# Kernel tuning notes

Hardware: AMD Instinct MI355X
Metric: run time of the kernel (lower is better)

## Reference

```python
import jax, jax.numpy as jnp
import numpy as np

B, T, C, U = 128, 160, 6000, 32
BLANK = C - 1          # Keras ctc_batch_cost / tf.nn.ctc_loss: blank is last class
S = 2 * U + 1          # extended label length (blanks interleaved)
NEG = -1e30
EPS = 1e-7             # keras.backend.epsilon()


def setup_inputs() -> dict:
    key = jax.random.key(0)
    k1, k2, k3, k4 = jax.random.split(key, 4)
    logits = jax.random.normal(k1, (B, T, C), dtype=jnp.float32)
    y_pred = jax.nn.softmax(logits, axis=-1)  # ctc_batch_cost expects probabilities
    y_true = jax.random.randint(k2, (B, U), 0, C - 1)      # labels exclude blank
    input_length = jax.random.randint(k3, (B, 1), 120, T + 1)
    label_length = jax.random.randint(k4, (B, 1), 8, U + 1)
    return {"y_true": y_true, "y_pred": y_pred,
            "input_length": input_length, "label_length": label_length}


def _ctc_batch_cost(y_true, y_pred, input_length, label_length):
    # log probs, matching K.ctc_batch_cost: log(y_pred + epsilon)
    log_probs = jnp.log(y_pred + EPS)                      # [B,T,C]

    # extended label sequence: blank, l1, blank, l2, ..., blank
    ext = jnp.full((B, S), BLANK, dtype=y_true.dtype).at[:, 1::2].set(y_true)  # [B,S]
    # skip transition s-2 -> s allowed iff ext[s] != blank and ext[s] != ext[s-2]
    skip = jnp.zeros((B, S), dtype=bool)
    skip = skip.at[:, 3::2].set(y_true[:, 1:] != y_true[:, :-1])

    # per-frame log prob of each extended symbol: [B,T,S]
    lp_ext = jnp.take_along_axis(log_probs, ext[:, None, :], axis=2)

    # alpha at t=0: only positions 0 (blank) and 1 (first label)
    alpha0 = (jnp.full((B, S), NEG, dtype=log_probs.dtype)
              .at[:, 0].set(lp_ext[:, 0, 0])
              .at[:, 1].set(lp_ext[:, 0, 1]))

    def step(alpha, x):
        lp_t, t = x                                        # lp_t: [B,S]
        p1 = jnp.pad(alpha, ((0, 0), (1, 0)), constant_values=NEG)[:, :S]
        p2 = jnp.pad(alpha, ((0, 0), (2, 0)), constant_values=NEG)[:, :S]
        new = jnp.logaddexp(jnp.logaddexp(alpha, p1),
                            jnp.where(skip, p2, NEG)) + lp_t
        # freeze sequences that have run out of frames
        new = jnp.where(t < input_length, new, alpha)
        return new, None

    lp_seq = jnp.swapaxes(lp_ext, 0, 1)[1:]                # [T-1,B,S]
    ts = jnp.arange(1, T)
    alpha, _ = jax.lax.scan(step, alpha0, (lp_seq, ts))

    # total prob ends at final blank (s=2L) or final label (s=2L-1)
    end = 2 * label_length                                  # [B,1]
    a_end = jnp.take_along_axis(alpha, end, axis=1)[:, 0]
    a_end1 = jnp.take_along_axis(alpha, end - 1, axis=1)[:, 0]
    loss = -jnp.logaddexp(a_end, a_end1)
    return loss[:, None]                                    # [B,1], as in Keras


def reference(y_true, y_pred, input_length, label_length):
    return _ctc_batch_cost(y_true, y_pred, input_length, label_length)
```

## Files before the change

### kernel.cpp

```cpp
#include <hip/hip_runtime.h>
#include <math.h>

#define BB 128
#define TT 160
#define CC 6000
#define UU 32
#define SS 65
#define BLANK (CC - 1)
#define NEGV (-1e30f)
#define EPSV (1e-7f)
#define NTHR 1024

__device__ __forceinline__ float laddexp(float a, float b) {
    float m = fmaxf(a, b);
    float d = fabsf(a - b);
    return m + log1pf(expf(-d));
}

__global__ __launch_bounds__(NTHR) void ctc_loss_kernel(
    const int*   __restrict__ y_true,
    const float* __restrict__ y_pred,
    const int*   __restrict__ input_length,
    const int*   __restrict__ label_length,
    float*       __restrict__ out)
{
    __shared__ float lpb[TT];
    __shared__ float lpl[TT * UU];
    __shared__ int   yt[UU];

    const int b   = blockIdx.x;
    const int tid = threadIdx.x;

    if (tid < UU) yt[tid] = y_true[b * UU + tid];
    __syncthreads();

    const int len = input_length[b];
    const int L   = label_length[b];

    const float* yp = y_pred + (size_t)b * TT * CC;
    for (int t = tid; t < len; t += NTHR)
        lpb[t] = logf(yp[t * CC + BLANK] + EPSV);
    const int nl = len * UU;
    for (int idx = tid; idx < nl; idx += NTHR) {
        int t = idx >> 5;
        int u = idx & 31;
        lpl[idx] = logf(yp[t * CC + yt[u]] + EPSV);
    }
    __syncthreads();

    if (tid >= 64) return;
    const int  lane = tid;
    const bool odd  = lane & 1;
    const int  u    = lane >> 1;

    const bool skip = odd && (lane >= 3) && (yt[u] != yt[u - 1]);

    {
        float v0 = odd ? lpl[0] : lpb[0];
        float a = (lane <= 1) ? v0 : NEGV;
        float a64 = NEGV;

        float lpB_cur = lpb[1];
        float lp_cur  = odd ? lpl[UU + u] : lpB_cur;

        for (int t = 1; t < len; ++t) {
            int tn = (t + 1 < len) ? t + 1 : t;
            float lpB_nxt = lpb[tn];
            float lp_nxt  = odd ? lpl[tn * UU + u] : lpB_nxt;

            float a63 = __shfl(a, 63);
            float p1  = __shfl_up(a, 1);
            float p2  = __shfl_up(a, 2);
            if (lane < 1) p1 = NEGV;
            if (lane < 2) p2 = NEGV;

            float nv  = laddexp(laddexp(a, p1), skip ? p2 : NEGV) + lp_cur;
            float n64 = laddexp(a64, a63) + lpB_cur;

            a   = nv;
            a64 = n64;
            lp_cur  = lp_nxt;
            lpB_cur = lpB_nxt;
        }

        const int e = 2 * L;
        float ae  = (e == 64) ? a64 : __shfl(a, e);
        float ae1 = __shfl(a, e - 1);

        if (lane == 0) out[b] = -laddexp(ae, ae1);
    }
}

extern "C" void kernel_launch(void* const* d_in, const int* in_sizes, int n_in,
                              void* d_out, int out_size, void* d_ws, size_t ws_size,
                              hipStream_t stream) {
    const int*   y_true       = (const int*)  d_in[0];
    const float* y_pred       = (const float*)d_in[1];
    const int*   input_length = (const int*)  d_in[2];
    const int*   label_length = (const int*)  d_in[3];
    float*       out          = (float*)      d_out;

    ctc_loss_kernel<<<BB, NTHR, 0, stream>>>(y_true, y_pred, input_length, label_length, out);
}
```

Measured before the change: 659.9 us.

## Split gather into a grid-wide kernel and prefetch two steps in DP

Moves the scattered log-prob gather out of the per-batch block into a separate kernel with one thread per (b,t,symbol), writing to a workspace buffer. The DP kernel then loads the compact table into shared memory and deepens the register prefetch to two time steps. This is meant to spread the latency-bound gather across many more blocks than the 128 per-sequence blocks. In exchange it adds a second launch and a global workspace round trip.

```diff
diff --git a/kernel.cpp b/kernel.cpp
--- a/kernel.cpp
+++ b/kernel.cpp
@@ -5,11 +5,11 @@
 #define TT 160
 #define CC 6000
 #define UU 32
-#define SS 65
+#define S33 33
 #define BLANK (CC - 1)
 #define NEGV (-1e30f)
 #define EPSV (1e-7f)
-#define NTHR 1024
+
 
 __device__ __forceinline__ float laddexp(float a, float b) {
     float m = fmaxf(a, b);
@@ -17,78 +17,85 @@
     return m + log1pf(expf(-d));
 }
 
-__global__ __launch_bounds__(NTHR) void ctc_loss_kernel(
+__global__ __launch_bounds__(256) void ctc_gather_kernel(
     const int*   __restrict__ y_true,
     const float* __restrict__ y_pred,
     const int*   __restrict__ input_length,
+    float*       __restrict__ lp)
+{
+    const int id = blockIdx.x * 256 + threadIdx.x;
+    const int s  = id % S33;
+    const int bt = id / S33;
+    const int t  = bt % TT;
+    const int b  = bt / TT;
+
+    if (t >= input_length[b]) return;
+
+    const int cls = (s == 32) ? BLANK : y_true[b * UU + s];
+    const float v = y_pred[((size_t)b * TT + t) * CC + cls];
+    lp[id] = logf(v + EPSV);
+}
+
+__global__ __launch_bounds__(256) void ctc_dp_kernel(
+    const int*   __restrict__ y_true,
+    const int*   __restrict__ input_length,
     const int*   __restrict__ label_length,
+    const float* __restrict__ lp,
     float*       __restrict__ out)
 {
-    __shared__ float lpb[TT];
-    __shared__ float lpl[TT * UU];
-    __shared__ int   yt[UU];
+    __shared__ float sl[TT * S33];
 
     const int b   = blockIdx.x;
     const int tid = threadIdx.x;
-
-    if (tid < UU) yt[tid] = y_true[b * UU + tid];
-    __syncthreads();
-
     const int len = input_length[b];
     const int L   = label_length[b];
 
-    const float* yp = y_pred + (size_t)b * TT * CC;
-    for (int t = tid; t < len; t += NTHR)
-        lpb[t] = logf(yp[t * CC + BLANK] + EPSV);
-    const int nl = len * UU;
-    for (int idx = tid; idx < nl; idx += NTHR) {
-        int t = idx >> 5;
-        int u = idx & 31;
-        lpl[idx] = logf(yp[t * CC + yt[u]] + EPSV);
-    }
+    const float* src = lp + (size_t)b * TT * S33;
+    const int n = len * S33;
+    for (int i = tid; i < n; i += 256) sl[i] = src[i];
     __syncthreads();
 
     if (tid >= 64) return;
     const int  lane = tid;
     const bool odd  = lane & 1;
     const int  u    = lane >> 1;
+    const int  col  = odd ? u : 32;
 
-    const bool skip = odd && (lane >= 3) && (yt[u] != yt[u - 1]);
+    bool skip = false;
+    if (odd && lane >= 3)
+        skip = y_true[b * UU + u] != y_true[b * UU + u - 1];
 
-    {
-        float v0 = odd ? lpl[0] : lpb[0];
-        float a = (lane <= 1) ? v0 : NEGV;
-        float a64 = NEGV;
+    float a   = (lane == 0) ? sl[32] : (lane == 1) ? sl[0] : NEGV;
+    float a64 = NEGV;
 
-        float lpB_cur = lpb[1];
-        float lp_cur  = odd ? lpl[UU + u] : lpB_cur;
+    float c0 = sl[1 * S33 + col], c0B = sl[1 * S33 + 32];
+    float c1 = sl[2 * S33 + col], c1B = sl[2 * S33 + 32];
 
-        for (int t = 1; t < len; ++t) {
-            int tn = (t + 1 < len) ? t + 1 : t;
-            float lpB_nxt = lpb[tn];
-            float lp_nxt  = odd ? lpl[tn * UU + u] : lpB_nxt;
+    for (int t = 1; t < len; ++t) {
+        int tp = t + 2; if (tp >= len) tp = len - 1;
+        float nl = sl[tp * S33 + col];
+        float nB = sl[tp * S33 + 32];
 
-            float a63 = __shfl(a, 63);
-            float p1  = __shfl_up(a, 1);
-            float p2  = __shfl_up(a, 2);
-            if (lane < 1) p1 = NEGV;
-            if (lane < 2) p2 = NEGV;
+        float a63 = __shfl(a, 63);
+        float p1  = __shfl_up(a, 1);
+        float p2  = __shfl_up(a, 2);
+        if (lane < 1) p1 = NEGV;
+        if (lane < 2) p2 = NEGV;
 
-            float nv  = laddexp(laddexp(a, p1), skip ? p2 : NEGV) + lp_cur;
-            float n64 = laddexp(a64, a63) + lpB_cur;
+        float nv  = laddexp(laddexp(a, p1), skip ? p2 : NEGV) + c0;
+        float n64 = laddexp(a64, a63) + c0B;
 
-            a   = nv;
-            a64 = n64;
-            lp_cur  = lp_nxt;
-            lpB_cur = lpB_nxt;
-        }
+        a   = nv;
+        a64 = n64;
+        c0 = c1; c0B = c1B;
+        c1 = nl; c1B = nB;
+    }
 
-        const int e = 2 * L;
-        float ae  = (e == 64) ? a64 : __shfl(a, e);
-        float ae1 = __shfl(a, e - 1);
+    const int e = 2 * L;
+    float ae  = (e == 64) ? a64 : __shfl(a, e);
+    float ae1 = __shfl(a, e - 1);
 
-        if (lane == 0) out[b] = -laddexp(ae, ae1);
-    }
+    if (lane == 0) out[b] = -laddexp(ae, ae1);
 }
 
 extern "C" void kernel_launch(void* const* d_in, const int* in_sizes, int n_in,
@@ -99,6 +106,9 @@
     const int*   input_length = (const int*)  d_in[2];
     const int*   label_length = (const int*)  d_in[3];
     float*       out          = (float*)      d_out;
+    float*       lp           = (float*)      d_ws;
 
-    ctc_loss_kernel<<<BB, NTHR, 0, stream>>>(y_true, y_pred, input_length, label_length, out);
+    const int total = BB * TT * S33;
+    ctc_gather_kernel<<<total / 256, 256, 0, stream>>>(y_true, y_pred, input_length, lp);
+    ctc_dp_kernel<<<BB, 256, 0, stream>>>(y_true, input_length, label_length, lp, out);
 }
```

Result: no change. 657.5 us (-0.4%).
